# Optimization experiments

Measured on AMD Instinct MI355X. Metric: run time of the kernel, lower is better.

## Reference

```python
import jax, jax.numpy as jnp
import numpy as np
from jax import lax

WINDOW_SIZE = 11
SIGMA = 1.5
C1 = 0.01 ** 2
C2 = 0.03 ** 2


def _gaussian_window(window_size, sigma, channel):
    # 1D gaussian, normalized, then outer product -> 2D window
    x = np.arange(window_size) - window_size // 2
    g = np.exp(-(x.astype(np.float64) ** 2) / (2.0 * sigma ** 2))
    g = (g / g.sum()).astype(np.float32)
    w2d = np.outer(g, g)  # [K, K]
    # depthwise kernel [C, 1, K, K] (OIHW with feature_group_count=C)
    w = np.broadcast_to(w2d, (channel, 1, window_size, window_size))
    return jnp.asarray(np.ascontiguousarray(w))


def _depthwise_conv(x, w, channel):
    pad = WINDOW_SIZE // 2
    return lax.conv_general_dilated(
        x, w,
        window_strides=(1, 1),
        padding=[(pad, pad), (pad, pad)],
        dimension_numbers=("NCHW", "OIHW", "NCHW"),
        feature_group_count=channel,
    )


def setup_inputs() -> dict:
    key = jax.random.key(0)
    k1, k2 = jax.random.split(key)
    B, C, H, W = 32, 3, 512, 512
    img1 = jax.random.uniform(k1, (B, C, H, W), dtype=jnp.float32)
    img2 = jax.random.uniform(k2, (B, C, H, W), dtype=jnp.float32)
    return {"img1": img1, "img2": img2}


def reference(img1, img2):
    channel = img1.shape[1]
    window = _gaussian_window(WINDOW_SIZE, SIGMA, channel)

    mu1 = _depthwise_conv(img1, window, channel)
    mu2 = _depthwise_conv(img2, window, channel)

    mu1_sq = mu1 * mu1
    mu2_sq = mu2 * mu2
    mu1_mu2 = mu1 * mu2

    sigma1_sq = _depthwise_conv(img1 * img1, window, channel) - mu1_sq
    sigma2_sq = _depthwise_conv(img2 * img2, window, channel) - mu2_sq
    sigma12 = _depthwise_conv(img1 * img2, window, channel) - mu1_mu2

    sigma1_sq = jnp.maximum(sigma1_sq, 0.0)
    sigma2_sq = jnp.maximum(sigma2_sq, 0.0)

    numerator = (2.0 * mu1_mu2 + C1) * (2.0 * sigma12 + C2)
    denominator = (mu1_sq + mu2_sq + C1) * (sigma1_sq + sigma2_sq + C2)
    ssim_map = jnp.clip(numerator / denominator, 0.0, 1.0)

    return 1.0 - jnp.mean(ssim_map)
```

## Files before the change

kernel.cpp:

```cpp
#include <hip/hip_runtime.h>


typedef float v2f __attribute__((ext_vector_type(2)));
typedef float v4f __attribute__((ext_vector_type(4)));

constexpr int IMG    = 512;
constexpr int TPB    = 256;
constexpr int SH     = 64;
constexpr int NPAIR  = 37;
constexpr int LW     = 272;
constexpr int PLANES = 32 * 3;
constexpr int NBLK   = (IMG / TPB) * (IMG / SH) * PLANES;
constexpr double N_PIX = 25165824.0;

__global__ __launch_bounds__(TPB, 4) void ssim_map_kernel(
    const float* __restrict__ img1, const float* __restrict__ img2,
    double* __restrict__ partial)
{
    constexpr float GW[11] = {
        0.0010283801f, 0.0075987583f, 0.0360007721f, 0.1093607008f,
        0.2130055439f, 0.2660117257f, 0.2130055439f, 0.1093607008f,
        0.0360007721f, 0.0075987583f, 0.0010283801f };
    constexpr float GWp[13] = {
        0.0f,
        0.0010283801f, 0.0075987583f, 0.0360007721f, 0.1093607008f,
        0.2130055439f, 0.2660117257f, 0.2130055439f, 0.1093607008f,
        0.0360007721f, 0.0075987583f, 0.0010283801f,
        0.0f };

    __shared__ v4f  sbuf[3][LW];
    __shared__ float wsum[TPB / 64];

    const int tid   = threadIdx.x;
    const int x0    = blockIdx.x * TPB;
    const int y0    = blockIdx.y * SH;
    const int plane = blockIdx.z;
    const bool yedge = (blockIdx.y == 0) || (blockIdx.y == (IMG / SH - 1));

    const float* p1 = img1 + (size_t)plane * IMG * IMG;
    const float* p2 = img2 + (size_t)plane * IMG * IMG;

    const int  c    = x0 + tid - 8;
    const bool cok  = (unsigned)c < (unsigned)IMG;
    const int  cc   = cok ? c : 0;
    const int  c2   = x0 + 248 + tid;
    const bool c2ok = (unsigned)c2 < (unsigned)IMG;
    const int  cc2  = c2ok ? c2 : 0;

    v2f rg1[6], rg2[6], rg11[6], rg22[6], rg12[6];
    v2f accv = {0.0f, 0.0f};

    float pa1, pb1, pa2, pb2, qa1, qb1, qa2, qb2;

    auto prefetch_g = [&](int i) {
        const int  rA  = y0 - 5 + 2 * i;
        const int  rB  = rA + 1;
        const bool aok = (unsigned)rA < (unsigned)IMG;
        const bool bok = (unsigned)rB < (unsigned)IMG;
        const size_t oA = (size_t)rA * IMG;
        const size_t oB = (size_t)rB * IMG;
        pa1 = (aok && cok) ? p1[oA + cc] : 0.0f;
        pb1 = (bok && cok) ? p1[oB + cc] : 0.0f;
        pa2 = (aok && cok) ? p2[oA + cc] : 0.0f;
        pb2 = (bok && cok) ? p2[oB + cc] : 0.0f;
        if (tid < 16) {
            qa1 = (aok && c2ok) ? p1[oA + cc2] : 0.0f;
            qb1 = (bok && c2ok) ? p1[oB + cc2] : 0.0f;
            qa2 = (aok && c2ok) ? p2[oA + cc2] : 0.0f;
            qb2 = (bok && c2ok) ? p2[oB + cc2] : 0.0f;
        }
    };
    auto prefetch_f = [&](int i) {
        const size_t oA = (size_t)(y0 - 5 + 2 * i) * IMG;
        const size_t oB = oA + IMG;
        pa1 = cok ? p1[oA + cc] : 0.0f;
        pb1 = cok ? p1[oB + cc] : 0.0f;
        pa2 = cok ? p2[oA + cc] : 0.0f;
        pb2 = cok ? p2[oB + cc] : 0.0f;
        if (tid < 16) {
            qa1 = c2ok ? p1[oA + cc2] : 0.0f;
            qb1 = c2ok ? p1[oB + cc2] : 0.0f;
            qa2 = c2ok ? p2[oA + cc2] : 0.0f;
            qb2 = c2ok ? p2[oB + cc2] : 0.0f;
        }
    };

    if (yedge) prefetch_g(0); else prefetch_f(0);

    for (int ib = 0; ib < NPAIR; ib += 6) {
#pragma unroll
        for (int j = 0; j < 6; ++j) {
            const int i = ib + j;
            if (i < NPAIR) {
                sbuf[j % 3][tid] = v4f{pa1, pb1, pa2, pb2};
                if (tid < 16) sbuf[j % 3][256 + tid] = v4f{qa1, qb1, qa2, qb2};

                if (i + 1 < NPAIR) {
                    if (yedge) prefetch_g(i + 1); else prefetch_f(i + 1);
                }

                __syncthreads();

                v2f a1 = {0,0}, a2 = {0,0}, a11 = {0,0}, a22 = {0,0}, a12 = {0,0};
                const v4f* sp = &sbuf[j % 3][tid + 3];
#pragma unroll
                for (int k = 0; k < 11; ++k) {
                    const v4f s  = sp[k];
                    const v2f x1 = __builtin_shufflevector(s, s, 0, 1);
                    const v2f x2 = __builtin_shufflevector(s, s, 2, 3);
                    const float g = GW[k];
                    const v2f t1 = g * x1;
                    const v2f t2 = g * x2;
                    a1 += t1;
                    a2 += t2;
                    a11 = __builtin_elementwise_fma(t1, x1, a11);
                    a22 = __builtin_elementwise_fma(t2, x2, a22);
                    a12 = __builtin_elementwise_fma(t1, x2, a12);
                }
                rg1[j] = a1;  rg2[j] = a2;
                rg11[j] = a11; rg22[j] = a22; rg12[j] = a12;
            }

            if (i >= 5 && i < NPAIR) {
                v2f sx1={0,0}, sy1={0,0}, sx2={0,0}, sy2={0,0};
                v2f sx11={0,0}, sy11={0,0}, sx22={0,0}, sy22={0,0};
                v2f sx12={0,0}, sy12={0,0};
#pragma unroll
                for (int m = 0; m < 6; ++m) {
                    const int s = (j + 1 + m) % 6;
                    const v2f wx = { GWp[2*m + 1], GWp[2*m + 2] };
                    const v2f wy = { GWp[2*m],     GWp[2*m + 1] };
                    sx1  = __builtin_elementwise_fma(wx, rg1[s],  sx1);
                    sy1  = __builtin_elementwise_fma(wy, rg1[s],  sy1);
                    sx2  = __builtin_elementwise_fma(wx, rg2[s],  sx2);
                    sy2  = __builtin_elementwise_fma(wy, rg2[s],  sy2);
                    sx11 = __builtin_elementwise_fma(wx, rg11[s], sx11);
                    sy11 = __builtin_elementwise_fma(wy, rg11[s], sy11);
                    sx22 = __builtin_elementwise_fma(wx, rg22[s], sx22);
                    sy22 = __builtin_elementwise_fma(wy, rg22[s], sy22);
                    sx12 = __builtin_elementwise_fma(wx, rg12[s], sx12);
                    sy12 = __builtin_elementwise_fma(wy, rg12[s], sy12);
                }
                const v2f m1  = { sx1.x + sx1.y,  sy1.x + sy1.y };
                const v2f m2  = { sx2.x + sx2.y,  sy2.x + sy2.y };
                const v2f e11 = { sx11.x + sx11.y, sy11.x + sy11.y };
                const v2f e22 = { sx22.x + sx22.y, sy22.x + sy22.y };
                const v2f e12 = { sx12.x + sx12.y, sy12.x + sy12.y };

                const v2f mu11 = m1 * m1;
                const v2f mu22 = m2 * m2;
                const v2f mu12 = m1 * m2;
                const v2f zero = {0.0f, 0.0f};
                const v2f one  = {1.0f, 1.0f};
                const v2f sg1  = __builtin_elementwise_max(e11 - mu11, zero);
                const v2f sg2  = __builtin_elementwise_max(e22 - mu22, zero);
                const v2f sg12 = e12 - mu12;
                const v2f num = (2.0f * mu12 + 1e-4f) * (2.0f * sg12 + 9e-4f);
                const v2f den = (mu11 + mu22 + 1e-4f) * (sg1 + sg2 + 9e-4f);
                v2f v = { num.x * __builtin_amdgcn_rcpf(den.x),
                          num.y * __builtin_amdgcn_rcpf(den.y) };
                v = __builtin_elementwise_min(__builtin_elementwise_max(v, zero), one);
                accv += v;
            }
        }
    }

    float acc = accv.x + accv.y;
#pragma unroll
    for (int off = 32; off > 0; off >>= 1)
        acc += __shfl_down(acc, off, 64);
    if ((tid & 63) == 0) wsum[tid >> 6] = acc;
    __syncthreads();
    if (tid == 0) {
        double blocksum = 0.0;
#pragma unroll
        for (int w = 0; w < TPB / 64; ++w) blocksum += (double)wsum[w];
        const int bid = blockIdx.x + (IMG / TPB) * (blockIdx.y + (IMG / SH) * blockIdx.z);
        partial[bid] = blocksum;
    }
}

__global__ __launch_bounds__(256) void ssim_finalize_kernel(
    const double* __restrict__ partial, float* __restrict__ out)
{
    __shared__ double wsum[4];
    const int tid = threadIdx.x;
    double s = 0.0;
#pragma unroll
    for (int k = 0; k < NBLK / 256; ++k) s += partial[tid + 256 * k];
#pragma unroll
    for (int off = 32; off > 0; off >>= 1)
        s += __shfl_down(s, off, 64);
    if ((tid & 63) == 0) wsum[tid >> 6] = s;
    __syncthreads();
    if (tid == 0) {
        double t = wsum[0] + wsum[1] + wsum[2] + wsum[3];
        out[0] = 1.0f - (float)(t / N_PIX);
    }
}

extern "C" void kernel_launch(void* const* d_in, const int* in_sizes, int n_in,
                              void* d_out, int out_size, void* d_ws, size_t ws_size,
                              hipStream_t stream) {
    const float* img1 = (const float*)d_in[0];
    const float* img2 = (const float*)d_in[1];
    float* out = (float*)d_out;
    double* parts = (double*)d_ws;

    dim3 grid(IMG / TPB, IMG / SH, PLANES);
    ssim_map_kernel<<<grid, TPB, 0, stream>>>(img1, img2, parts);
    ssim_finalize_kernel<<<1, 256, 0, stream>>>(parts, out);
}
```

Before: 261.4 us.

## Process two columns per thread with even/odd LDS split covering full row width

Each block now covers a full 512-wide row strip, and each thread handles two adjacent columns. Rows are loaded with float2 and de-interleaved into even and odd LDS arrays, which zero-padded halo entries replace. This removes the x-halo reload (272 vs 256 columns), the second halo load path, and the edge-specific branches. The cost is doubled register state per thread (launch bounds lowered to 2 waves) and half as many blocks, which may reduce occupancy and latency hiding.

```diff
diff --git a/kernel.cpp b/kernel.cpp
--- a/kernel.cpp
+++ b/kernel.cpp
@@ -8,12 +8,12 @@
 constexpr int TPB    = 256;
 constexpr int SH     = 64;
 constexpr int NPAIR  = 37;
-constexpr int LW     = 272;
+constexpr int LW     = 264;
 constexpr int PLANES = 32 * 3;
-constexpr int NBLK   = (IMG / TPB) * (IMG / SH) * PLANES;
+constexpr int NBLK   = (IMG / SH) * PLANES;
 constexpr double N_PIX = 25165824.0;
 
-__global__ __launch_bounds__(TPB, 4) void ssim_map_kernel(
+__global__ __launch_bounds__(TPB, 2) void ssim_map_kernel(
     const float* __restrict__ img1, const float* __restrict__ img2,
     double* __restrict__ partial)
 {
@@ -28,139 +28,142 @@
         0.0360007721f, 0.0075987583f, 0.0010283801f,
         0.0f };
 
-    __shared__ v4f  sbuf[3][LW];
+    __shared__ v4f  sE[3][LW];
+    __shared__ v4f  sO[3][LW];
     __shared__ float wsum[TPB / 64];
 
     const int tid   = threadIdx.x;
-    const int x0    = blockIdx.x * TPB;
-    const int y0    = blockIdx.y * SH;
-    const int plane = blockIdx.z;
-    const bool yedge = (blockIdx.y == 0) || (blockIdx.y == (IMG / SH - 1));
+    const int y0    = blockIdx.x * SH;
+    const int plane = blockIdx.y;
 
     const float* p1 = img1 + (size_t)plane * IMG * IMG;
     const float* p2 = img2 + (size_t)plane * IMG * IMG;
 
-    const int  c    = x0 + tid - 8;
-    const bool cok  = (unsigned)c < (unsigned)IMG;
-    const int  cc   = cok ? c : 0;
-    const int  c2   = x0 + 248 + tid;
-    const bool c2ok = (unsigned)c2 < (unsigned)IMG;
-    const int  cc2  = c2ok ? c2 : 0;
-
-    v2f rg1[6], rg2[6], rg11[6], rg22[6], rg12[6];
+    if (tid < 48) {
+        const int b = tid >> 4, r = tid & 15, arr = r >> 3, p = r & 7;
+        const int idx = (p < 4) ? p : (256 + p);
+        if (arr) sO[b][idx] = v4f{0.f, 0.f, 0.f, 0.f};
+        else     sE[b][idx] = v4f{0.f, 0.f, 0.f, 0.f};
+    }
+
+    v2f rA1[6], rA2[6], rA11[6], rA22[6], rA12[6];
+    v2f rB1[6], rB2[6], rB11[6], rB22[6], rB12[6];
     v2f accv = {0.0f, 0.0f};
 
-    float pa1, pb1, pa2, pb2, qa1, qb1, qa2, qb2;
-
-    auto prefetch_g = [&](int i) {
+    float2 pa1, pb1, pa2, pb2;
+    const int c0 = 2 * tid;
+
+    auto prefetch = [&](int i) {
         const int  rA  = y0 - 5 + 2 * i;
         const int  rB  = rA + 1;
         const bool aok = (unsigned)rA < (unsigned)IMG;
         const bool bok = (unsigned)rB < (unsigned)IMG;
-        const size_t oA = (size_t)rA * IMG;
-        const size_t oB = (size_t)rB * IMG;
-        pa1 = (aok && cok) ? p1[oA + cc] : 0.0f;
-        pb1 = (bok && cok) ? p1[oB + cc] : 0.0f;
-        pa2 = (aok && cok) ? p2[oA + cc] : 0.0f;
-        pb2 = (bok && cok) ? p2[oB + cc] : 0.0f;
-        if (tid < 16) {
-            qa1 = (aok && c2ok) ? p1[oA + cc2] : 0.0f;
-            qb1 = (bok && c2ok) ? p1[oB + cc2] : 0.0f;
-            qa2 = (aok && c2ok) ? p2[oA + cc2] : 0.0f;
-            qb2 = (bok && c2ok) ? p2[oB + cc2] : 0.0f;
-        }
+        const size_t oA = aok ? (size_t)rA * IMG : 0;
+        const size_t oB = bok ? (size_t)rB * IMG : 0;
+        pa1 = *(const float2*)(p1 + oA + c0);
+        pb1 = *(const float2*)(p1 + oB + c0);
+        pa2 = *(const float2*)(p2 + oA + c0);
+        pb2 = *(const float2*)(p2 + oB + c0);
+        if (!aok) { pa1 = make_float2(0.f, 0.f); pa2 = make_float2(0.f, 0.f); }
+        if (!bok) { pb1 = make_float2(0.f, 0.f); pb2 = make_float2(0.f, 0.f); }
     };
-    auto prefetch_f = [&](int i) {
-        const size_t oA = (size_t)(y0 - 5 + 2 * i) * IMG;
-        const size_t oB = oA + IMG;
-        pa1 = cok ? p1[oA + cc] : 0.0f;
-        pb1 = cok ? p1[oB + cc] : 0.0f;
-        pa2 = cok ? p2[oA + cc] : 0.0f;
-        pb2 = cok ? p2[oB + cc] : 0.0f;
-        if (tid < 16) {
-            qa1 = c2ok ? p1[oA + cc2] : 0.0f;
-            qb1 = c2ok ? p1[oB + cc2] : 0.0f;
-            qa2 = c2ok ? p2[oA + cc2] : 0.0f;
-            qb2 = c2ok ? p2[oB + cc2] : 0.0f;
-        }
-    };
-
-    if (yedge) prefetch_g(0); else prefetch_f(0);
+
+    prefetch(0);
 
     for (int ib = 0; ib < NPAIR; ib += 6) {
 #pragma unroll
         for (int j = 0; j < 6; ++j) {
             const int i = ib + j;
+            const int s = j % 3;
             if (i < NPAIR) {
-                sbuf[j % 3][tid] = v4f{pa1, pb1, pa2, pb2};
-                if (tid < 16) sbuf[j % 3][256 + tid] = v4f{qa1, qb1, qa2, qb2};
-
-                if (i + 1 < NPAIR) {
-                    if (yedge) prefetch_g(i + 1); else prefetch_f(i + 1);
+                sE[s][tid + 4] = v4f{pa1.x, pb1.x, pa2.x, pb2.x};
+                sO[s][tid + 4] = v4f{pa1.y, pb1.y, pa2.y, pb2.y};
+
+                if (i + 1 < NPAIR) prefetch(i + 1);
+
+                __syncthreads();
+
+                const v4f* eb = &sE[s][tid + 2];
+                const v4f* ob = &sO[s][tid + 1];
+                v2f a1A={0,0}, a2A={0,0}, a11A={0,0}, a22A={0,0}, a12A={0,0};
+                v2f a1B={0,0}, a2B={0,0}, a11B={0,0}, a22B={0,0}, a12B={0,0};
+#pragma unroll
+                for (int k = 0; k < 11; ++k) {
+                    const float g = GW[k];
+                    const v4f sA = (k & 1) ? eb[(k - 1) >> 1] : ob[k >> 1];
+                    const v4f sB = (k & 1) ? ob[(k + 1) >> 1] : eb[k >> 1];
+                    {   const v2f x1 = __builtin_shufflevector(sA, sA, 0, 1);
+                        const v2f x2 = __builtin_shufflevector(sA, sA, 2, 3);
+                        const v2f t1 = g * x1;
+                        const v2f t2 = g * x2;
+                        a1A += t1; a2A += t2;
+                        a11A = __builtin_elementwise_fma(t1, x1, a11A);
+                        a22A = __builtin_elementwise_fma(t2, x2, a22A);
+                        a12A = __builtin_elementwise_fma(t1, x2, a12A); }
+                    {   const v2f x1 = __builtin_shufflevector(sB, sB, 0, 1);
+                        const v2f x2 = __builtin_shufflevector(sB, sB, 2, 3);
+                        const v2f t1 = g * x1;
+                        const v2f t2 = g * x2;
+                        a1B += t1; a2B += t2;
+                        a11B = __builtin_elementwise_fma(t1, x1, a11B);
+                        a22B = __builtin_elementwise_fma(t2, x2, a22B);
+                        a12B = __builtin_elementwise_fma(t1, x2, a12B); }
                 }
-
-                __syncthreads();
-
-                v2f a1 = {0,0}, a2 = {0,0}, a11 = {0,0}, a22 = {0,0}, a12 = {0,0};
-                const v4f* sp = &sbuf[j % 3][tid + 3];
-#pragma unroll
-                for (int k = 0; k < 11; ++k) {
-                    const v4f s  = sp[k];
-                    const v2f x1 = __builtin_shufflevector(s, s, 0, 1);
-                    const v2f x2 = __builtin_shufflevector(s, s, 2, 3);
-                    const float g = GW[k];
-                    const v2f t1 = g * x1;
-                    const v2f t2 = g * x2;
-                    a1 += t1;
-                    a2 += t2;
-                    a11 = __builtin_elementwise_fma(t1, x1, a11);
-                    a22 = __builtin_elementwise_fma(t2, x2, a22);
-                    a12 = __builtin_elementwise_fma(t1, x2, a12);
+                rA1[j] = a1A;  rA2[j] = a2A;  rA11[j] = a11A;
+                rA22[j] = a22A; rA12[j] = a12A;
+                rB1[j] = a1B;  rB2[j] = a2B;  rB11[j] = a11B;
+                rB22[j] = a22B; rB12[j] = a12B;
+            }
+
+            if (i >= 5 && i < NPAIR) {
+#pragma unroll
+                for (int col = 0; col < 2; ++col) {
+                    const v2f* g1  = col ? rB1  : rA1;
+                    const v2f* g2  = col ? rB2  : rA2;
+                    const v2f* g11 = col ? rB11 : rA11;
+                    const v2f* g22 = col ? rB22 : rA22;
+                    const v2f* g12 = col ? rB12 : rA12;
+                    v2f sx1={0,0}, sy1={0,0}, sx2={0,0}, sy2={0,0};
+                    v2f sx11={0,0}, sy11={0,0}, sx22={0,0}, sy22={0,0};
+                    v2f sx12={0,0}, sy12={0,0};
+#pragma unroll
+                    for (int m = 0; m < 6; ++m) {
+                        const int q = (j + 1 + m) % 6;
+                        const v2f wx = { GWp[2*m + 1], GWp[2*m + 2] };
+                        const v2f wy = { GWp[2*m],     GWp[2*m + 1] };
+                        sx1  = __builtin_elementwise_fma(wx, g1[q],  sx1);
+                        sy1  = __builtin_elementwise_fma(wy, g1[q],  sy1);
+                        sx2  = __builtin_elementwise_fma(wx, g2[q],  sx2);
+                        sy2  = __builtin_elementwise_fma(wy, g2[q],  sy2);
+                        sx11 = __builtin_elementwise_fma(wx, g11[q], sx11);
+                        sy11 = __builtin_elementwise_fma(wy, g11[q], sy11);
+                        sx22 = __builtin_elementwise_fma(wx, g22[q], sx22);
+                        sy22 = __builtin_elementwise_fma(wy, g22[q], sy22);
+                        sx12 = __builtin_elementwise_fma(wx, g12[q], sx12);
+                        sy12 = __builtin_elementwise_fma(wy, g12[q], sy12);
+                    }
+                    const v2f m1  = { sx1.x + sx1.y,  sy1.x + sy1.y };
+                    const v2f m2  = { sx2.x + sx2.y,  sy2.x + sy2.y };
+                    const v2f e11 = { sx11.x + sx11.y, sy11.x + sy11.y };
+                    const v2f e22 = { sx22.x + sx22.y, sy22.x + sy22.y };
+                    const v2f e12 = { sx12.x + sx12.y, sy12.x + sy12.y };
+
+                    const v2f mu11 = m1 * m1;
+                    const v2f mu22 = m2 * m2;
+                    const v2f mu12 = m1 * m2;
+                    const v2f zero = {0.0f, 0.0f};
+                    const v2f one  = {1.0f, 1.0f};
+                    const v2f sg1  = __builtin_elementwise_max(e11 - mu11, zero);
+                    const v2f sg2  = __builtin_elementwise_max(e22 - mu22, zero);
+                    const v2f sg12 = e12 - mu12;
+                    const v2f num = (2.0f * mu12 + 1e-4f) * (2.0f * sg12 + 9e-4f);
+                    const v2f den = (mu11 + mu22 + 1e-4f) * (sg1 + sg2 + 9e-4f);
+                    v2f v = { num.x * __builtin_amdgcn_rcpf(den.x),
+                              num.y * __builtin_amdgcn_rcpf(den.y) };
+                    v = __builtin_elementwise_min(
+                            __builtin_elementwise_max(v, zero), one);
+                    accv += v;
                 }
-                rg1[j] = a1;  rg2[j] = a2;
-                rg11[j] = a11; rg22[j] = a22; rg12[j] = a12;
-            }
-
-            if (i >= 5 && i < NPAIR) {
-                v2f sx1={0,0}, sy1={0,0}, sx2={0,0}, sy2={0,0};
-                v2f sx11={0,0}, sy11={0,0}, sx22={0,0}, sy22={0,0};
-                v2f sx12={0,0}, sy12={0,0};
-#pragma unroll
-                for (int m = 0; m < 6; ++m) {
-                    const int s = (j + 1 + m) % 6;
-                    const v2f wx = { GWp[2*m + 1], GWp[2*m + 2] };
-                    const v2f wy = { GWp[2*m],     GWp[2*m + 1] };
-                    sx1  = __builtin_elementwise_fma(wx, rg1[s],  sx1);
-                    sy1  = __builtin_elementwise_fma(wy, rg1[s],  sy1);
-                    sx2  = __builtin_elementwise_fma(wx, rg2[s],  sx2);
-                    sy2  = __builtin_elementwise_fma(wy, rg2[s],  sy2);
-                    sx11 = __builtin_elementwise_fma(wx, rg11[s], sx11);
-                    sy11 = __builtin_elementwise_fma(wy, rg11[s], sy11);
-                    sx22 = __builtin_elementwise_fma(wx, rg22[s], sx22);
-                    sy22 = __builtin_elementwise_fma(wy, rg22[s], sy22);
-                    sx12 = __builtin_elementwise_fma(wx, rg12[s], sx12);
-                    sy12 = __builtin_elementwise_fma(wy, rg12[s], sy12);
-                }
-                const v2f m1  = { sx1.x + sx1.y,  sy1.x + sy1.y };
-                const v2f m2  = { sx2.x + sx2.y,  sy2.x + sy2.y };
-                const v2f e11 = { sx11.x + sx11.y, sy11.x + sy11.y };
-                const v2f e22 = { sx22.x + sx22.y, sy22.x + sy22.y };
-                const v2f e12 = { sx12.x + sx12.y, sy12.x + sy12.y };
-
-                const v2f mu11 = m1 * m1;
-                const v2f mu22 = m2 * m2;
-                const v2f mu12 = m1 * m2;
-                const v2f zero = {0.0f, 0.0f};
-                const v2f one  = {1.0f, 1.0f};
-                const v2f sg1  = __builtin_elementwise_max(e11 - mu11, zero);
-                const v2f sg2  = __builtin_elementwise_max(e22 - mu22, zero);
-                const v2f sg12 = e12 - mu12;
-                const v2f num = (2.0f * mu12 + 1e-4f) * (2.0f * sg12 + 9e-4f);
-                const v2f den = (mu11 + mu22 + 1e-4f) * (sg1 + sg2 + 9e-4f);
-                v2f v = { num.x * __builtin_amdgcn_rcpf(den.x),
-                          num.y * __builtin_amdgcn_rcpf(den.y) };
-                v = __builtin_elementwise_min(__builtin_elementwise_max(v, zero), one);
-                accv += v;
             }
         }
     }
@@ -175,7 +178,7 @@
         double blocksum = 0.0;
 #pragma unroll
         for (int w = 0; w < TPB / 64; ++w) blocksum += (double)wsum[w];
-        const int bid = blockIdx.x + (IMG / TPB) * (blockIdx.y + (IMG / SH) * blockIdx.z);
+        const int bid = blockIdx.x + (IMG / SH) * blockIdx.y;
         partial[bid] = blocksum;
     }
 }
@@ -207,7 +210,7 @@
     float* out = (float*)d_out;
     double* parts = (double*)d_ws;
 
-    dim3 grid(IMG / TPB, IMG / SH, PLANES);
+    dim3 grid(IMG / SH, PLANES);
     ssim_map_kernel<<<grid, TPB, 0, stream>>>(img1, img2, parts);
     ssim_finalize_kernel<<<1, 256, 0, stream>>>(parts, out);
 }
```

After: 267.0 us. 2.2% more time.
